# Performance work log

Measured on AMD Instinct MI355X. Metric: run time of the kernel, lower is better.

The kernel has to match this reference:

```python
import jax, jax.numpy as jnp
import numpy as np
from jax import lax

B, C, HW = 8, 512, 32
NH = 8            # num_heads
NG = 32           # num_groups
HD = C // NH      # head_size = 64
EPS = 1e-6


def group_norm(x, gamma, beta, groups=NG, eps=EPS):
    b, c, h, w = x.shape
    xr = x.reshape(b, groups, c // groups, h, w)
    mu = xr.mean(axis=(2, 3, 4), keepdims=True)
    var = xr.var(axis=(2, 3, 4), keepdims=True)
    xn = ((xr - mu) / jnp.sqrt(var + eps)).reshape(b, c, h, w)
    return xn * gamma[None, :, None, None] + beta[None, :, None, None]


def conv2d(x, w, b):
    y = lax.conv_general_dilated(x, w, (1, 1), 'SAME',
                                 dimension_numbers=('NCHW', 'OIHW', 'NCHW'))
    return y + b[None, :, None, None]


def setup_inputs() -> dict:
    key = jax.random.key(0)
    ks = jax.random.split(key, 24)
    f32 = jnp.float32

    def lin(k, out_d, in_d):
        return (jax.random.normal(k, (out_d, in_d), f32) / np.sqrt(in_d)).astype(f32)

    inp = {
        'hidden_states': jax.random.normal(ks[0], (B, C, HW, HW), f32),
        'pre_g': jnp.ones(C, f32), 'pre_b': jnp.zeros(C, f32),
        'norm_g': jnp.ones(C, f32), 'norm_b': jnp.zeros(C, f32),
        'post_g': jnp.ones(C, f32), 'post_b': jnp.zeros(C, f32),
        'pos_emb': jax.random.normal(ks[1], (1, C, 32, 32), f32) * 0.02,
        'sa_w1': (jax.random.normal(ks[2], (C // 8, C, 1, 1), f32) / np.sqrt(C)),
        'sa_b1': jnp.zeros(C // 8, f32),
        'sa_w2': (jax.random.normal(ks[3], (C // 8, C // 8, 3, 3), f32) / np.sqrt(9 * C // 8)),
        'sa_b2': jnp.zeros(C // 8, f32),
        'sa_w3': (jax.random.normal(ks[4], (1, C // 8, 1, 1), f32) / np.sqrt(C // 8)),
        'sa_b3': jnp.zeros(1, f32),
        'wq': lin(ks[5], C, C), 'wk': lin(ks[6], C, C), 'wv': lin(ks[7], C, C),
        'wq0': lin(ks[8], C // 2, C), 'wk0': lin(ks[9], C // 2, C), 'wv0': lin(ks[10], C // 2, C),
        'wq1': lin(ks[11], C // 2, C), 'wk1': lin(ks[12], C // 2, C), 'wv1': lin(ks[13], C // 2, C),
        'ff_w1': lin(ks[14], C, 2 * C), 'ff_b1': jnp.zeros(C, f32),
        'ff_w2': lin(ks[15], C, C), 'ff_b2': jnp.zeros(C, f32),
        'out_w': lin(ks[16], C, C), 'out_b': jnp.zeros(C, f32),
    }
    return inp


def reference(hidden_states, pre_g, pre_b, norm_g, norm_b, post_g, post_b,
              pos_emb, sa_w1, sa_b1, sa_w2, sa_b2, sa_w3, sa_b3,
              wq, wk, wv, wq0, wk0, wv0, wq1, wk1, wv1,
              ff_w1, ff_b1, ff_w2, ff_b2, out_w, out_b):
    b, c, h, w = hidden_states.shape
    S = h * w
    residual = hidden_states

    hs = group_norm(hidden_states, pre_g, pre_b)
    # H=W=32 matches pos_embedding; bilinear resize to same size is identity
    hs = hs + pos_emb

    # spatial attention gating (conv 1x1 -> SiLU -> conv 3x3 -> SiLU -> conv 1x1 -> sigmoid)
    a = jax.nn.silu(conv2d(hs, sa_w1, sa_b1))
    a = jax.nn.silu(conv2d(a, sa_w2, sa_b2))
    spatial_weights = jax.nn.sigmoid(conv2d(a, sa_w3, sa_b3))
    spatial_enhanced = hs * spatial_weights

    # standard multi-head self-attention over flattened tokens
    sh = group_norm(hs, norm_g, norm_b).reshape(b, c, S).transpose(0, 2, 1)  # (B,S,C)
    ehs = sh  # encoder_hidden_states defaults to standard_hidden

    q = (sh @ wq.T).reshape(b, S, NH, HD)
    k = (ehs @ wk.T).reshape(b, S, NH, HD)
    v = (ehs @ wv.T).reshape(b, S, NH, HD)
    scores = jnp.einsum('bqhd,bkhd->bhqk', q, k) / np.sqrt(HD)
    probs = jax.nn.softmax(scores, axis=-1)
    std_out = jnp.einsum('bhqk,bkhd->bqhd', probs, v).reshape(b, S, c)

    # two multi-scale single-head attention branches (dim C/2 each)
    msh = spatial_enhanced.reshape(b, c, S).transpose(0, 2, 1)  # (B,S,C)
    parts = []
    for wqm, wkm, wvm in ((wq0, wk0, wv0), (wq1, wk1, wv1)):
        qm = msh @ wqm.T          # (B,S,C/2)
        km = ehs @ wkm.T
        vm = ehs @ wvm.T
        sc = jnp.einsum('bqd,bkd->bqk', qm, km) / np.sqrt(c // 2)
        parts.append(jnp.einsum('bqk,bkd->bqd', jax.nn.softmax(sc, axis=-1), vm))
    multi_out = jnp.concatenate(parts, axis=-1)  # (B,S,C)

    combined = jnp.concatenate([std_out, multi_out], axis=-1)  # (B,S,2C)
    fused = jax.nn.silu(combined @ ff_w1.T + ff_b1) @ ff_w2.T + ff_b2  # dropout = eval identity
    final = fused @ out_w.T + out_b
    final = final.transpose(0, 2, 1).reshape(b, c, h, w)
    final = group_norm(final, post_g, post_b)
    return final + residual
```

## Files before the change

kernel.cpp:

```cpp
#include <hip/hip_runtime.h>
#include <hip/hip_bf16.h>
#include <math.h>

typedef __attribute__((ext_vector_type(8))) __bf16 v8bf;
typedef __attribute__((ext_vector_type(4))) float v4f;

__device__ __forceinline__ unsigned short f2bf(float f) {
  union { float f; unsigned int u; } a; a.f = f;
  unsigned int r = a.u + 0x7fffu + ((a.u >> 16) & 1u);
  return (unsigned short)(r >> 16);
}
__device__ __forceinline__ unsigned short f2bf_trunc(float f) {
  union { float f; unsigned int u; } a; a.f = f;
  return (unsigned short)(a.u >> 16);
}
__device__ __forceinline__ float bf2f(unsigned short u) {
  union { unsigned int i; float f; } a; a.i = ((unsigned int)u) << 16; return a.f;
}
__device__ __forceinline__ float sigm(float x) { return 1.0f / (1.0f + __expf(-x)); }

__device__ __forceinline__ void async16(const void* g, void* l) {
  __builtin_amdgcn_global_load_lds(
      (const __attribute__((address_space(1))) unsigned int*)g,
      (__attribute__((address_space(3))) unsigned int*)l, 16, 0, 0);
}

__global__ __launch_bounds__(256) void gn_pre_kernel(
    const float* __restrict__ x, const float* __restrict__ g, const float* __restrict__ be,
    const float* __restrict__ pos, unsigned short* __restrict__ hsb, float* __restrict__ stats) {
  __shared__ float L[16384];
  __shared__ float rs[4], rs2[4], mr[2];
  int b = blockIdx.x >> 5, grp = blockIdx.x & 31;
  const float4* base = (const float4*)(x + ((size_t)b*512 + grp*16)*1024);
  float4* L4 = (float4*)L;
  int w = threadIdx.x >> 6;
  float s = 0.f, s2 = 0.f;
  for (int i = threadIdx.x; i < 4096; i += 256) {
    float4 v = base[i];
    L4[i] = v;
    s += v.x + v.y + v.z + v.w;
    s2 += v.x*v.x + v.y*v.y + v.z*v.z + v.w*v.w;
  }
#pragma unroll
  for (int o = 32; o; o >>= 1) { s += __shfl_xor(s, o); s2 += __shfl_xor(s2, o); }
  if ((threadIdx.x & 63) == 0) { rs[w] = s; rs2[w] = s2; }
  __syncthreads();
  if (threadIdx.x == 0) {
    float ts = rs[0]+rs[1]+rs[2]+rs[3], ts2 = rs2[0]+rs2[1]+rs2[2]+rs2[3];
    float mu = ts * (1.0f/16384.0f);
    float var = ts2 * (1.0f/16384.0f) - mu*mu;
    mr[0] = mu; mr[1] = rsqrtf(var + 1e-6f);
  }
  __syncthreads();
  float mu = mr[0], rstd = mr[1];
  const float4* pb = (const float4*)(pos + (size_t)grp*16*1024);
  float ns = 0.f, ns2 = 0.f;
  for (int i = threadIdx.x; i < 4096; i += 256) {
    float4 v = L4[i], p = pb[i];
    int c = grp*16 + (i >> 8);
    float gg = g[c], bb = be[c];
    float4 o;
    o.x = (v.x - mu)*rstd*gg + bb + p.x;
    o.y = (v.y - mu)*rstd*gg + bb + p.y;
    o.z = (v.z - mu)*rstd*gg + bb + p.z;
    o.w = (v.w - mu)*rstd*gg + bb + p.w;
    L4[i] = o;
    ns += o.x + o.y + o.z + o.w;
    ns2 += o.x*o.x + o.y*o.y + o.z*o.z + o.w*o.w;
  }
#pragma unroll
  for (int o = 32; o; o >>= 1) { ns += __shfl_xor(ns, o); ns2 += __shfl_xor(ns2, o); }
  if ((threadIdx.x & 63) == 0) { rs[w] = ns; rs2[w] = ns2; }
  __syncthreads();
  if (threadIdx.x == 0) {
    float ts = rs[0]+rs[1]+rs[2]+rs[3], ts2 = rs2[0]+rs2[1]+rs2[2]+rs2[3];
    float nmu = ts * (1.0f/16384.0f);
    float nvar = ts2 * (1.0f/16384.0f) - nmu*nmu;
    stats[(b*32+grp)*2] = nmu; stats[(b*32+grp)*2+1] = rsqrtf(nvar + 1e-6f);
  }
#pragma unroll
  for (int j = 0; j < 4; ++j) {
    int sI = threadIdx.x + j*256;
    unsigned int wd[8];
#pragma unroll
    for (int c = 0; c < 8; ++c) {
      unsigned int lo = f2bf(L[(2*c)*1024 + sI]);
      unsigned int hi = f2bf(L[(2*c+1)*1024 + sI]);
      wd[c] = lo | (hi << 16);
    }
    size_t oo = (size_t)(b*1024 + sI)*512 + grp*16;
    *(uint4*)(hsb + oo)     = make_uint4(wd[0], wd[1], wd[2], wd[3]);
    *(uint4*)(hsb + oo + 8) = make_uint4(wd[4], wd[5], wd[6], wd[7]);
  }
}

__global__ __launch_bounds__(256) void im2col_kernel(
    const unsigned short* __restrict__ a1, unsigned short* __restrict__ im2) {
  int row0 = blockIdx.x * 8;
#pragma unroll
  for (int it = 0; it < 3; ++it) {
    int cc = it*256 + threadIdx.x;
    if (cc >= 576) break;
    int rl = cc / 72, rr = cc - rl*72;
    int tap = rr >> 3, ch8 = rr & 7;
    int row = row0 + rl;
    int bb = row >> 10, s = row & 1023;
    int y = s >> 5, xx0 = s & 31;
    int yy = y + tap/3 - 1, xx = xx0 + tap%3 - 1;
    ushort4 v0 = make_ushort4(0,0,0,0), v1 = make_ushort4(0,0,0,0);
    if ((unsigned)yy < 32u && (unsigned)xx < 32u) {
      const unsigned short* src = a1 + ((size_t)(bb*1024 + yy*32 + xx))*64 + ch8*8;
      v0 = *(const ushort4*)src; v1 = *(const ushort4*)(src + 4);
    }
    unsigned short* dst = im2 + (size_t)row*576 + tap*64 + ch8*8;
    *(ushort4*)dst = v0; *(ushort4*)(dst + 4) = v1;
  }
}

__global__ __launch_bounds__(256) void gate_norm_kernel(
    const unsigned short* __restrict__ hsb, const unsigned short* __restrict__ a2,
    const float* __restrict__ w3, const float* __restrict__ b3,
    const float* __restrict__ stats, const float* __restrict__ g,
    const float* __restrict__ be,
    unsigned short* __restrict__ sh, unsigned short* __restrict__ msh) {
  int b = blockIdx.y;
  int s = blockIdx.x * 4 + (threadIdx.x >> 6);
  int oct = threadIdx.x & 63;
  int c0 = oct * 8;
  int grp = c0 >> 4;
  float part = bf2f(a2[((size_t)(b*1024) + s)*64 + oct]) * w3[oct];
#pragma unroll
  for (int o = 32; o; o >>= 1) part += __shfl_xor(part, o);
  float wgt = sigm(part + b3[0]);
  float mu = stats[(b*32 + grp)*2], rstd = stats[(b*32 + grp)*2 + 1];
  size_t o = (size_t)(b*1024 + s)*512 + c0;
  ushort4 u0 = *(const ushort4*)(hsb + o), u1 = *(const ushort4*)(hsb + o + 4);
  unsigned short uu[8] = {u0.x,u0.y,u0.z,u0.w,u1.x,u1.y,u1.z,u1.w};
  unsigned short so[8], mo[8];
#pragma unroll
  for (int j = 0; j < 8; ++j) {
    float v = bf2f(uu[j]);
    so[j] = f2bf((v - mu)*rstd*g[c0+j] + be[c0+j]);
    mo[j] = f2bf(v * wgt);
  }
  *(ushort4*)(sh + o)     = make_ushort4(so[0], so[1], so[2], so[3]);
  *(ushort4*)(sh + o + 4) = make_ushort4(so[4], so[5], so[6], so[7]);
  *(ushort4*)(msh + o)     = make_ushort4(mo[0], mo[1], mo[2], mo[3]);
  *(ushort4*)(msh + o + 4) = make_ushort4(mo[4], mo[5], mo[6], mo[7]);
}

struct WCvt { const float* src; int dstOff; int n; float scale; };
struct WCvtArgs { WCvt w[14]; };
__global__ __launch_bounds__(256) void wconvert_kernel(WCvtArgs a, unsigned short* __restrict__ dst) {
  WCvt e = a.w[blockIdx.y];
  int i = blockIdx.x * 256 + threadIdx.x;
  if (i >= e.n) return;
  if (blockIdx.y == 13) {
    int oc = i / 576, r = i - oc*576;
    int tap = r >> 6, ic = r & 63;
    dst[e.dstOff + i] = f2bf(e.src[(oc*64 + ic)*9 + tap]);
  } else {
    dst[e.dstOff + i] = f2bf(e.src[i] * e.scale);
  }
}

__global__ __launch_bounds__(256) void transpose2_kernel(
    const unsigned short* __restrict__ qkvm,
    unsigned short* __restrict__ vtb, unsigned short* __restrict__ vmt) {
  __shared__ unsigned short t[64][65];
  int s0 = blockIdx.x * 64, c0 = blockIdx.y * 64;
  int z = blockIdx.z, b = z & 7;
  const unsigned short* in = qkvm + (z >= 8 ? 2048 : 1024);
  unsigned short* out = (z >= 8) ? vmt : vtb;
  int tx = threadIdx.x & 63, ty = threadIdx.x >> 6;
#pragma unroll
  for (int i = 0; i < 16; ++i) {
    int s = ty + i*4;
    t[s][tx] = in[((size_t)(b*1024 + s0 + s))*2560 + c0 + tx];
  }
  __syncthreads();
#pragma unroll
  for (int i = 0; i < 16; ++i) {
    int c = ty + i*4;
    out[((size_t)b*512 + c0 + c)*1024 + s0 + tx] = t[tx][c];
  }
}

struct GemmDesc {
  const unsigned short* A; const unsigned short* B; void* out; const float* bias;
  int M, N, K, lda, ldb, ldo, epi;
  long long Ay, Az, By, Bz, Oy, Oz;
};

template<int BM, int BN>
__global__ __launch_bounds__(256) void gemm_tile_kernel(GemmDesc d) {
  constexpr int WGM = (BN >= 128) ? 2 : 4;
  constexpr int WGN = 4 / WGM;
  constexpr int MT = BM / (16 * WGM);
  constexpr int NT = BN / (16 * WGN);
  constexpr int AIT = (BM * 4) / 256;
  constexpr int BIT = (BN * 4) / 256;
  __shared__ __align__(16) unsigned short As[BM * 32];
  __shared__ __align__(16) unsigned short Bs[BN * 32];

  int ntx = d.N / BN;
  int bm0 = (blockIdx.x / ntx) * BM, bn0 = (blockIdx.x % ntx) * BN;
  const unsigned short* A = d.A + (long long)blockIdx.y * d.Ay
      + (long long)blockIdx.z * d.Az + (size_t)bm0 * d.lda;
  const unsigned short* B = d.B + (long long)blockIdx.y * d.By
      + (long long)blockIdx.z * d.Bz + (size_t)bn0 * d.ldb;
  int tid = threadIdx.x, lane = tid & 63, w = tid >> 6;
  int wm = (WGN == 2) ? (w >> 1) : w;
  int wn = (WGN == 2) ? (w & 1) : 0;
  int ln = lane & 15, qd = lane >> 4;

  v4f acc[MT][NT];
#pragma unroll
  for (int i = 0; i < MT; ++i)
#pragma unroll
    for (int j = 0; j < NT; ++j) acc[i][j] = (v4f){0.f, 0.f, 0.f, 0.f};

  int nks = d.K >> 5;
  for (int ks = 0; ks < nks; ++ks) {
    int kof = ks * 32;
#pragma unroll
    for (int it = 0; it < AIT; ++it) {
      int c = it * 256 + tid;
      async16(A + (size_t)(c >> 2) * d.lda + (c & 3) * 8 + kof,
              As + (it * 256 + w * 64) * 8);
    }
#pragma unroll
    for (int it = 0; it < BIT; ++it) {
      int c = it * 256 + tid;
      async16(B + (size_t)(c >> 2) * d.ldb + (c & 3) * 8 + kof,
              Bs + (it * 256 + w * 64) * 8);
    }
    __syncthreads();
    v8bf af[MT], bfr[NT];
#pragma unroll
    for (int i = 0; i < MT; ++i)
      af[i] = *(const v8bf*)(As + (wm * MT * 16 + i * 16 + ln) * 32 + qd * 8);
#pragma unroll
    for (int j = 0; j < NT; ++j)
      bfr[j] = *(const v8bf*)(Bs + (wn * NT * 16 + j * 16 + ln) * 32 + qd * 8);
#pragma unroll
    for (int i = 0; i < MT; ++i)
#pragma unroll
      for (int j = 0; j < NT; ++j)
        acc[i][j] = __builtin_amdgcn_mfma_f32_16x16x32_bf16(af[i], bfr[j], acc[i][j], 0, 0, 0);
    __syncthreads();
  }

  size_t obase = (size_t)((long long)blockIdx.y * d.Oy + (long long)blockIdx.z * d.Oz);
#pragma unroll
  for (int i = 0; i < MT; ++i) {
#pragma unroll
    for (int j = 0; j < NT; ++j) {
      int col = bn0 + wn * NT * 16 + j * 16 + ln;
      float bia = d.bias ? d.bias[col] : 0.0f;
#pragma unroll
      for (int r = 0; r < 4; ++r) {
        int row = bm0 + wm * MT * 16 + i * 16 + qd * 4 + r;
        float v = acc[i][j][r] + bia;
        if (d.epi == 2) v = v * sigm(v);
        size_t oi = obase + (size_t)row * d.ldo + col;
        if (d.epi == 0) ((float*)d.out)[oi] = v;
        else ((unsigned short*)d.out)[oi] = f2bf(v);
      }
    }
  }
}

__global__ __launch_bounds__(256) void flash_attn_kernel(
    const unsigned short* __restrict__ QKVM, const unsigned short* __restrict__ VTB,
    unsigned short* __restrict__ out) {
  __shared__ __align__(16) unsigned short Ks[128*64];
  __shared__ __align__(16) unsigned short Vts[64*128];
  __shared__ __align__(16) unsigned short Pw[4][16*128];
  int h = blockIdx.x, b = blockIdx.y, qt = blockIdx.z;
  int tid = threadIdx.x, lane = tid & 63, w = tid >> 6;
  int ln = lane & 15, qd = lane >> 4;

  const unsigned short* Qbase = QKVM + ((size_t)(b*1024 + qt*128 + w*32))*2560 + h*64;
  v8bf aq[2][2];
#pragma unroll
  for (int i = 0; i < 2; ++i)
#pragma unroll
    for (int s = 0; s < 2; ++s)
      aq[i][s] = *(const v8bf*)(Qbase + (size_t)(i*16 + ln)*2560 + s*32 + qd*8);

  v4f o_acc[2][4];
  float l_part[2][4];
#pragma unroll
  for (int i = 0; i < 2; ++i)
#pragma unroll
    for (int dn = 0; dn < 4; ++dn) o_acc[i][dn] = (v4f){0.f,0.f,0.f,0.f};
#pragma unroll
  for (int i = 0; i < 2; ++i)
#pragma unroll
    for (int r = 0; r < 4; ++r) l_part[i][r] = 0.f;

  const unsigned short* Kg = QKVM + 512 + (size_t)(b*1024)*2560 + h*64;
  const unsigned short* Vg = VTB + ((size_t)(b*512) + h*64)*1024;

  for (int kt = 0; kt < 8; ++kt) {
#pragma unroll
    for (int it = 0; it < 4; ++it) {
      int c = it*256 + tid;
      async16(Kg + (size_t)(kt*128 + (c >> 3))*2560 + (((c & 7) ^ ((c >> 3) & 7)) << 3),
              Ks + c*8);
    }
#pragma unroll
    for (int it = 0; it < 4; ++it) {
      int c = it*256 + tid;
      async16(Vg + (size_t)(c >> 4)*1024 + kt*128 + ((((c & 15) ^ ((c >> 4) & 7))) << 3),
              Vts + c*8);
    }
    __syncthreads();

#pragma unroll
    for (int i = 0; i < 2; ++i) {
      v4f sc[8];
#pragma unroll
      for (int n = 0; n < 8; ++n) {
        v4f a = (v4f){0.f,0.f,0.f,0.f};
#pragma unroll
        for (int s = 0; s < 2; ++s) {
          v8bf kb = *(const v8bf*)(Ks + (n*16 + ln)*64 + (((s*4 + qd) ^ (ln & 7)) << 3));
          a = __builtin_amdgcn_mfma_f32_16x16x32_bf16(aq[i][s], kb, a, 0, 0, 0);
        }
        sc[n] = a;
      }
#pragma unroll
      for (int r = 0; r < 4; ++r) {
        int row7 = (qd*4 + r) & 7;
        float acc_l = 0.f;
#pragma unroll
        for (int n = 0; n < 8; ++n) {
          float p = exp2f(sc[n][r]);
          acc_l += p;
          Pw[w][(qd*4 + r)*128 + (((n*2 + (ln >> 3)) ^ row7) << 3) + (ln & 7)] = f2bf_trunc(p);
        }
        l_part[i][r] += acc_l;
      }
#pragma unroll
      for (int dn = 0; dn < 4; ++dn) {
        v4f a = o_acc[i][dn];
#pragma unroll
        for (int ks2 = 0; ks2 < 4; ++ks2) {
          int phys = (((ks2*4 + qd) ^ (ln & 7)) << 3);
          v8bf pf = *(const v8bf*)(&Pw[w][ln*128 + phys]);
          v8bf vf = *(const v8bf*)(Vts + (dn*16 + ln)*128 + phys);
          a = __builtin_amdgcn_mfma_f32_16x16x32_bf16(pf, vf, a, 0, 0, 0);
        }
        o_acc[i][dn] = a;
      }
    }
    __syncthreads();
  }

  unsigned short* ob = out + ((size_t)(b*1024 + qt*128 + w*32))*1024 + h*64;
#pragma unroll
  for (int i = 0; i < 2; ++i)
#pragma unroll
    for (int r = 0; r < 4; ++r) {
      float l = l_part[i][r];
      l += __shfl_xor(l, 1); l += __shfl_xor(l, 2);
      l += __shfl_xor(l, 4); l += __shfl_xor(l, 8);
      float rinv = 1.0f / l;
#pragma unroll
      for (int dn = 0; dn < 4; ++dn)
        ob[(size_t)(i*16 + qd*4 + r)*1024 + dn*16 + ln] = f2bf(o_acc[i][dn][r] * rinv);
    }
}

__global__ __launch_bounds__(256) void softmax_bf16_kernel(
    const unsigned short* __restrict__ S, unsigned short* __restrict__ P, int nrows) {
  int row = blockIdx.x * 4 + (threadIdx.x >> 6);
  if (row >= nrows) return;
  int l = threadIdx.x & 63;
  const ushort4* sp = (const ushort4*)(S + (size_t)row * 1024);
  float v[16];
  float m = -1e30f;
#pragma unroll
  for (int t = 0; t < 4; ++t) {
    ushort4 u = sp[t*64 + l];
    v[t*4+0] = bf2f(u.x); v[t*4+1] = bf2f(u.y); v[t*4+2] = bf2f(u.z); v[t*4+3] = bf2f(u.w);
    m = fmaxf(m, fmaxf(fmaxf(v[t*4], v[t*4+1]), fmaxf(v[t*4+2], v[t*4+3])));
  }
#pragma unroll
  for (int o = 32; o; o >>= 1) m = fmaxf(m, __shfl_xor(m, o));
  float sum = 0.f;
#pragma unroll
  for (int t = 0; t < 16; ++t) { v[t] = __expf(v[t] - m); sum += v[t]; }
#pragma unroll
  for (int o = 32; o; o >>= 1) sum += __shfl_xor(sum, o);
  float r = 1.0f / sum;
  ushort4* p = (ushort4*)(P + (size_t)row * 1024);
#pragma unroll
  for (int t = 0; t < 4; ++t)
    p[t*64 + l] = make_ushort4(f2bf_trunc(v[t*4]*r), f2bf_trunc(v[t*4+1]*r),
                               f2bf_trunc(v[t*4+2]*r), f2bf_trunc(v[t*4+3]*r));
}

__global__ __launch_bounds__(256) void gn_stats_bf16_kernel(
    const unsigned short* __restrict__ t, float* __restrict__ stats) {
  int b = blockIdx.x >> 5, grp = blockIdx.x & 31;
  float s = 0.f, s2 = 0.f;
#pragma unroll
  for (int j = 0; j < 4; ++j) {
    int sI = threadIdx.x + j*256;
    const unsigned short* p = t + ((size_t)(b*1024 + sI))*512 + grp*16;
    uint4 a = *(const uint4*)p, c2 = *(const uint4*)(p + 8);
    unsigned int ww[8] = {a.x,a.y,a.z,a.w,c2.x,c2.y,c2.z,c2.w};
#pragma unroll
    for (int k = 0; k < 8; ++k) {
      float lo = bf2f((unsigned short)(ww[k] & 0xffff));
      float hi = bf2f((unsigned short)(ww[k] >> 16));
      s += lo + hi; s2 += lo*lo + hi*hi;
    }
  }
#pragma unroll
  for (int o = 32; o; o >>= 1) { s += __shfl_xor(s, o); s2 += __shfl_xor(s2, o); }
  __shared__ float rs[4], rs2[4];
  int w = threadIdx.x >> 6;
  if ((threadIdx.x & 63) == 0) { rs[w] = s; rs2[w] = s2; }
  __syncthreads();
  if (threadIdx.x == 0) {
    float ts = rs[0]+rs[1]+rs[2]+rs[3], ts2 = rs2[0]+rs2[1]+rs2[2]+rs2[3];
    float mu = ts * (1.0f/16384.0f);
    float var = ts2 * (1.0f/16384.0f) - mu*mu;
    stats[(b*32+grp)*2] = mu; stats[(b*32+grp)*2+1] = rsqrtf(var + 1e-6f);
  }
}

__global__ __launch_bounds__(256) void final_out_kernel(
    const unsigned short* __restrict__ fin, const float* __restrict__ stats,
    const float* __restrict__ g, const float* __restrict__ be,
    const float* __restrict__ x, float* __restrict__ out) {
  __shared__ float t[64][65];
  int s0 = blockIdx.x * 64, c0 = blockIdx.y * 64, b = blockIdx.z;
  int tx = threadIdx.x & 63, ty = threadIdx.x >> 6;
#pragma unroll
  for (int i = 0; i < 16; ++i) {
    int s = ty + i*4;
    t[s][tx] = bf2f(fin[((size_t)(b*1024 + s0 + s))*512 + c0 + tx]);
  }
  __syncthreads();
#pragma unroll
  for (int i = 0; i < 16; ++i) {
    int c = ty + i*4;
    int cc = c0 + c, grp = cc >> 4;
    float mu = stats[(b*32+grp)*2], rstd = stats[(b*32+grp)*2+1];
    float gg = g[cc], bb = be[cc];
    size_t oi = ((size_t)(b*512 + cc))*1024 + s0 + tx;
    out[oi] = (t[tx][c] - mu)*rstd*gg + bb + x[oi];
  }
}

static void launch_gemm128(hipStream_t st, const unsigned short* A, const unsigned short* B,
                           void* out, const float* bias,
                           int M, int N, int K, int lda, int ldb, int ldo, int epi,
                           long long Ay, long long Az, long long By, long long Bz,
                           long long Oy, long long Oz, int gy, int gz) {
  GemmDesc d{A, B, out, bias, M, N, K, lda, ldb, ldo, epi, Ay, Az, By, Bz, Oy, Oz};
  gemm_tile_kernel<128,128><<<dim3((M/128)*(N/128), gy, gz), dim3(256), 0, st>>>(d);
}
static void launch_gemm64(hipStream_t st, const unsigned short* A, const unsigned short* B,
                          void* out, const float* bias,
                          int M, int N, int K, int lda, int ldb, int ldo, int epi) {
  GemmDesc d{A, B, out, bias, M, N, K, lda, ldb, ldo, epi, 0,0,0,0,0,0};
  gemm_tile_kernel<128,64><<<dim3((M/128)*(N/64), 1, 1), dim3(256), 0, st>>>(d);
}

extern "C" void kernel_launch(void* const* d_in, const int* in_sizes, int n_in,
                              void* d_out, int out_size, void* d_ws, size_t ws_size,
                              hipStream_t stream) {
  const float* x      = (const float*)d_in[0];
  const float* pre_g  = (const float*)d_in[1];
  const float* pre_b  = (const float*)d_in[2];
  const float* norm_g = (const float*)d_in[3];
  const float* norm_b = (const float*)d_in[4];
  const float* post_g = (const float*)d_in[5];
  const float* post_b = (const float*)d_in[6];
  const float* pos    = (const float*)d_in[7];
  const float* sa_b1  = (const float*)d_in[9];
  const float* sa_b2  = (const float*)d_in[11];
  const float* sa_w3  = (const float*)d_in[12];
  const float* sa_b3  = (const float*)d_in[13];
  const float* ff_b1  = (const float*)d_in[24];
  const float* ff_b2  = (const float*)d_in[26];
  const float* out_b  = (const float*)d_in[28];
  float* outp = (float*)d_out;

  char* ws = (char*)d_ws;
  size_t off = 0;
  auto alloc = [&](size_t bytes) -> void* {
    void* p = ws + off; off += (bytes + 255) & ~(size_t)255; return p;
  };
  float* STATS = (float*)alloc(4096);
  unsigned short* HSB  = (unsigned short*)alloc(8388608);
  unsigned short* A1   = (unsigned short*)alloc(1048576);
  unsigned short* IM2  = (unsigned short*)alloc(9437184);
  unsigned short* A2   = (unsigned short*)alloc(1048576);
  unsigned short* SHB  = (unsigned short*)alloc(8388608);
  unsigned short* MSHB = (unsigned short*)alloc(8388608);
  unsigned short* WBF  = (unsigned short*)alloc(6291456);
  unsigned short* QKVM = (unsigned short*)alloc(41943040);
  unsigned short* QM   = (unsigned short*)alloc(8388608);
  unsigned short* VTB  = (unsigned short*)alloc(8388608);
  unsigned short* VMT  = (unsigned short*)alloc(8388608);
  unsigned short* SBUF = (unsigned short*)alloc(16777216);
  unsigned short* PBUF = (unsigned short*)alloc(16777216);
  unsigned short* COMB = (unsigned short*)alloc(16777216);
  unsigned short* FFMID= (unsigned short*)alloc(8388608);
  unsigned short* FUSED= (unsigned short*)alloc(8388608);
  unsigned short* FINALB=(unsigned short*)alloc(8388608);

  const int OQKVM=0, OQM=1310720, OFF1=1572864, OFF2=2097152,
            OOW=2359296, OW1=2621440, OW2R=2654208;

  gn_pre_kernel<<<dim3(256), dim3(256), 0, stream>>>(x, pre_g, pre_b, pos, HSB, STATS);
  {
    WCvtArgs a;
    const float LG2E = 1.4426950408889634f;
    const int   srcIdx[14] = {14,15,16, 18,21,19,22, 17,20, 23,25,27, 8, 10};
    const int   dofs[14]   = {0, 262144, 524288,
                              786432, 917504, 1048576, 1179648,
                              OQM, OQM+131072,
                              OFF1, OFF2, OOW, OW1, OW2R};
    const int   ns[14]     = {262144,262144,262144, 131072,131072,131072,131072,
                              131072,131072, 524288,262144,262144, 32768, 36864};
    const float sc[14]     = {0.125f*LG2E,1.f,1.f, 1.f,1.f,1.f,1.f,
                              0.0625f,0.0625f, 1.f,1.f,1.f, 1.f, 1.f};
    for (int i = 0; i < 14; ++i) { a.w[i].src = (const float*)d_in[srcIdx[i]]; a.w[i].dstOff = dofs[i]; a.w[i].n = ns[i]; a.w[i].scale = sc[i]; }
    wconvert_kernel<<<dim3(2048, 14), dim3(256), 0, stream>>>(a, WBF);
  }
  launch_gemm64(stream, HSB, WBF+OW1,  A1, sa_b1, 8192, 64, 512, 512, 512, 64, 2);
  im2col_kernel<<<dim3(1024), dim3(256), 0, stream>>>(A1, IM2);
  launch_gemm64(stream, IM2, WBF+OW2R, A2, sa_b2, 8192, 64, 576, 576, 576, 64, 2);
  gate_norm_kernel<<<dim3(256, 8), dim3(256), 0, stream>>>(HSB, A2, sa_w3, sa_b3, STATS, norm_g, norm_b, SHB, MSHB);

  launch_gemm128(stream, SHB,  WBF+OQKVM, QKVM, nullptr, 8192, 2560, 512, 512, 512, 2560, 1, 0,0,0,0,0,0, 1,1);
  launch_gemm128(stream, MSHB, WBF+OQM,   QM,   nullptr, 8192, 512,  512, 512, 512, 512,  1, 0,0,0,0,0,0, 1,1);

  transpose2_kernel<<<dim3(16, 8, 16), dim3(256), 0, stream>>>(QKVM, VTB, VMT);

  flash_attn_kernel<<<dim3(8, 8, 8), dim3(256), 0, stream>>>(QKVM, VTB, COMB);

  for (int br = 0; br < 2; ++br) {
    launch_gemm128(stream, QM + br*256, QKVM + 1536 + br*256, SBUF, nullptr,
                   1024, 1024, 256, 512, 2560, 1024, 1,
                   1024LL*512, 0, 1024LL*2560, 0, 1024LL*1024, 0, 8, 1);
    softmax_bf16_kernel<<<dim3(2048), dim3(256), 0, stream>>>(SBUF, PBUF, 8192);
    launch_gemm128(stream, PBUF, VMT + (size_t)br*256*1024, COMB + 512 + br*256, nullptr,
                   1024, 256, 1024, 1024, 1024, 1024, 1,
                   1024LL*1024, 0, 512LL*1024, 0, 1024LL*1024, 0, 8, 1);
  }

  launch_gemm128(stream, COMB,  WBF+OFF1, FFMID,  ff_b1, 8192, 512, 1024, 1024, 1024, 512, 2, 0,0,0,0,0,0, 1,1);
  launch_gemm128(stream, FFMID, WBF+OFF2, FUSED,  ff_b2, 8192, 512, 512,  512,  512,  512, 1, 0,0,0,0,0,0, 1,1);
  launch_gemm128(stream, FUSED, WBF+OOW,  FINALB, out_b, 8192, 512, 512,  512,  512,  512, 1, 0,0,0,0,0,0, 1,1);

  gn_stats_bf16_kernel<<<dim3(256), dim3(256), 0, stream>>>(FINALB, STATS);
  final_out_kernel<<<dim3(16, 8, 8), dim3(256), 0, stream>>>(FINALB, STATS, post_g, post_b, x, outp);

  (void)in_sizes; (void)n_in; (void)out_size; (void)ws_size;
}
```

Measured before the change: 479.9 us.

## Fold ff_w2 and out_w into one weight, batch attention branches, XCD-aware tile mapping

Precomputes out_w·ff_w2 as a combined 512x512 weight and a folded bias, so the two back-to-back linear layers become a single GEMM over the activations. The two multi-scale attention branches are launched as one batched GEMM/softmax/GEMM sequence via the z grid dimension instead of a loop, halving launches. GEMM tiles are remapped so consecutive blocks on the same XCD share M rows for better L2 locality. This adds a small per-call weight GEMM, a bias kernel and larger score buffers, and the folded weight is rounded to bf16 once more.

Measured after the change: 457.3 us. -4.7%, faster.

```diff
diff --git a/kernel.cpp b/kernel.cpp
--- a/kernel.cpp
+++ b/kernel.cpp
@@ -150,7 +150,7 @@
 }
 
 struct WCvt { const float* src; int dstOff; int n; float scale; };
-struct WCvtArgs { WCvt w[14]; };
+struct WCvtArgs { WCvt w[15]; };
 __global__ __launch_bounds__(256) void wconvert_kernel(WCvtArgs a, unsigned short* __restrict__ dst) {
   WCvt e = a.w[blockIdx.y];
   int i = blockIdx.x * 256 + threadIdx.x;
@@ -159,9 +159,22 @@
     int oc = i / 576, r = i - oc*576;
     int tap = r >> 6, ic = r & 63;
     dst[e.dstOff + i] = f2bf(e.src[(oc*64 + ic)*9 + tap]);
+  } else if (blockIdx.y == 14) {
+    dst[e.dstOff + i] = f2bf(e.src[(i & 511)*512 + (i >> 9)]);
   } else {
     dst[e.dstOff + i] = f2bf(e.src[i] * e.scale);
   }
+}
+
+__global__ __launch_bounds__(256) void bias_fold_kernel(
+    const float* __restrict__ ow, const float* __restrict__ b2,
+    const float* __restrict__ ob, float* __restrict__ bc) {
+  int n = blockIdx.x * 256 + threadIdx.x;
+  float s = ob[n];
+  const float* r = ow + (size_t)n * 512;
+#pragma unroll 8
+  for (int j = 0; j < 512; ++j) s += r[j] * b2[j];
+  bc[n] = s;
 }
 
 __global__ __launch_bounds__(256) void transpose2_kernel(
@@ -203,8 +216,17 @@
   __shared__ __align__(16) unsigned short As[BM * 32];
   __shared__ __align__(16) unsigned short Bs[BN * 32];
 
-  int ntx = d.N / BN;
-  int bm0 = (blockIdx.x / ntx) * BM, bn0 = (blockIdx.x % ntx) * BN;
+  int ntx = d.N / BN, mtx = d.M / BM;
+  int bmt, bnt;
+  if ((mtx & 7) == 0) {
+    int xcd = blockIdx.x & 7, j = blockIdx.x >> 3;
+    int mpx = mtx >> 3;
+    bmt = xcd * mpx + (j % mpx);
+    bnt = j / mpx;
+  } else {
+    bmt = blockIdx.x / ntx; bnt = blockIdx.x % ntx;
+  }
+  int bm0 = bmt * BM, bn0 = bnt * BN;
   const unsigned short* A = d.A + (long long)blockIdx.y * d.Ay
       + (long long)blockIdx.z * d.Az + (size_t)bm0 * d.lda;
   const unsigned short* B = d.B + (long long)blockIdx.y * d.By
@@ -490,6 +512,7 @@
   const float* sa_b3  = (const float*)d_in[13];
   const float* ff_b1  = (const float*)d_in[24];
   const float* ff_b2  = (const float*)d_in[26];
+  const float* out_w  = (const float*)d_in[27];
   const float* out_b  = (const float*)d_in[28];
   float* outp = (float*)d_out;
 
@@ -499,6 +522,7 @@
     void* p = ws + off; off += (bytes + 255) & ~(size_t)255; return p;
   };
   float* STATS = (float*)alloc(4096);
+  float* BC    = (float*)alloc(2048);
   unsigned short* HSB  = (unsigned short*)alloc(8388608);
   unsigned short* A1   = (unsigned short*)alloc(1048576);
   unsigned short* IM2  = (unsigned short*)alloc(9437184);
@@ -506,36 +530,41 @@
   unsigned short* SHB  = (unsigned short*)alloc(8388608);
   unsigned short* MSHB = (unsigned short*)alloc(8388608);
   unsigned short* WBF  = (unsigned short*)alloc(6291456);
+  unsigned short* WCOMB= (unsigned short*)alloc(524288);
   unsigned short* QKVM = (unsigned short*)alloc(41943040);
   unsigned short* QM   = (unsigned short*)alloc(8388608);
   unsigned short* VTB  = (unsigned short*)alloc(8388608);
   unsigned short* VMT  = (unsigned short*)alloc(8388608);
-  unsigned short* SBUF = (unsigned short*)alloc(16777216);
-  unsigned short* PBUF = (unsigned short*)alloc(16777216);
+  unsigned short* SBUF = (unsigned short*)alloc(33554432);
+  unsigned short* PBUF = (unsigned short*)alloc(33554432);
   unsigned short* COMB = (unsigned short*)alloc(16777216);
   unsigned short* FFMID= (unsigned short*)alloc(8388608);
-  unsigned short* FUSED= (unsigned short*)alloc(8388608);
   unsigned short* FINALB=(unsigned short*)alloc(8388608);
 
-  const int OQKVM=0, OQM=1310720, OFF1=1572864, OFF2=2097152,
+  const int OQKVM=0, OQM=1310720, OFF1=1572864, OFF2T=2097152,
             OOW=2359296, OW1=2621440, OW2R=2654208;
 
   gn_pre_kernel<<<dim3(256), dim3(256), 0, stream>>>(x, pre_g, pre_b, pos, HSB, STATS);
   {
     WCvtArgs a;
     const float LG2E = 1.4426950408889634f;
-    const int   srcIdx[14] = {14,15,16, 18,21,19,22, 17,20, 23,25,27, 8, 10};
-    const int   dofs[14]   = {0, 262144, 524288,
+    const int   srcIdx[15] = {14,15,16, 18,21,19,22, 17,20, 23,27, 8, 0 , 10, 25};
+    const int   dofs[15]   = {0, 262144, 524288,
                               786432, 917504, 1048576, 1179648,
                               OQM, OQM+131072,
-                              OFF1, OFF2, OOW, OW1, OW2R};
-    const int   ns[14]     = {262144,262144,262144, 131072,131072,131072,131072,
-                              131072,131072, 524288,262144,262144, 32768, 36864};
-    const float sc[14]     = {0.125f*LG2E,1.f,1.f, 1.f,1.f,1.f,1.f,
-                              0.0625f,0.0625f, 1.f,1.f,1.f, 1.f, 1.f};
-    for (int i = 0; i < 14; ++i) { a.w[i].src = (const float*)d_in[srcIdx[i]]; a.w[i].dstOff = dofs[i]; a.w[i].n = ns[i]; a.w[i].scale = sc[i]; }
-    wconvert_kernel<<<dim3(2048, 14), dim3(256), 0, stream>>>(a, WBF);
-  }
+                              OFF1, OOW, OW1, 0, OW2R, OFF2T};
+    const int   ns[15]     = {262144,262144,262144, 131072,131072,131072,131072,
+                              131072,131072, 524288,262144, 32768, 0, 36864, 262144};
+    const float sc[15]     = {0.125f*LG2E,1.f,1.f, 1.f,1.f,1.f,1.f,
+                              0.0625f,0.0625f, 1.f,1.f, 1.f, 0.f, 1.f, 1.f};
+    for (int i = 0; i < 15; ++i) { a.w[i].src = (const float*)d_in[srcIdx[i]]; a.w[i].dstOff = dofs[i]; a.w[i].n = ns[i]; a.w[i].scale = sc[i]; }
+    wconvert_kernel<<<dim3(2048, 15), dim3(256), 0, stream>>>(a, WBF);
+  }
+  {
+    GemmDesc d{WBF+OOW, WBF+OFF2T, WCOMB, nullptr, 512, 512, 512, 512, 512, 512, 1, 0,0,0,0,0,0};
+    gemm_tile_kernel<128,128><<<dim3(16, 1, 1), dim3(256), 0, stream>>>(d);
+  }
+  bias_fold_kernel<<<dim3(2), dim3(256), 0, stream>>>(out_w, ff_b2, out_b, BC);
   launch_gemm64(stream, HSB, WBF+OW1,  A1, sa_b1, 8192, 64, 512, 512, 512, 64, 2);
   im2col_kernel<<<dim3(1024), dim3(256), 0, stream>>>(A1, IM2);
   launch_gemm64(stream, IM2, WBF+OW2R, A2, sa_b2, 8192, 64, 576, 576, 576, 64, 2);
@@ -548,19 +577,16 @@
 
   flash_attn_kernel<<<dim3(8, 8, 8), dim3(256), 0, stream>>>(QKVM, VTB, COMB);
 
-  for (int br = 0; br < 2; ++br) {
-    launch_gemm128(stream, QM + br*256, QKVM + 1536 + br*256, SBUF, nullptr,
-                   1024, 1024, 256, 512, 2560, 1024, 1,
-                   1024LL*512, 0, 1024LL*2560, 0, 1024LL*1024, 0, 8, 1);
-    softmax_bf16_kernel<<<dim3(2048), dim3(256), 0, stream>>>(SBUF, PBUF, 8192);
-    launch_gemm128(stream, PBUF, VMT + (size_t)br*256*1024, COMB + 512 + br*256, nullptr,
-                   1024, 256, 1024, 1024, 1024, 1024, 1,
-                   1024LL*1024, 0, 512LL*1024, 0, 1024LL*1024, 0, 8, 1);
-  }
+  launch_gemm128(stream, QM, QKVM + 1536, SBUF, nullptr,
+                 1024, 1024, 256, 512, 2560, 1024, 1,
+                 1024LL*512, 256, 1024LL*2560, 256, 1024LL*1024, 8388608, 8, 2);
+  softmax_bf16_kernel<<<dim3(4096), dim3(256), 0, stream>>>(SBUF, PBUF, 16384);
+  launch_gemm128(stream, PBUF, VMT, COMB + 512, nullptr,
+                 1024, 256, 1024, 1024, 1024, 1024, 1,
+                 1024LL*1024, 8388608, 512LL*1024, 256LL*1024, 1024LL*1024, 256, 8, 2);
 
   launch_gemm128(stream, COMB,  WBF+OFF1, FFMID,  ff_b1, 8192, 512, 1024, 1024, 1024, 512, 2, 0,0,0,0,0,0, 1,1);
-  launch_gemm128(stream, FFMID, WBF+OFF2, FUSED,  ff_b2, 8192, 512, 512,  512,  512,  512, 1, 0,0,0,0,0,0, 1,1);
-  launch_gemm128(stream, FUSED, WBF+OOW,  FINALB, out_b, 8192, 512, 512,  512,  512,  512, 1, 0,0,0,0,0,0, 1,1);
+  launch_gemm128(stream, FFMID, WCOMB,    FINALB, BC,    8192, 512, 512,  512,  512,  512, 1, 0,0,0,0,0,0, 1,1);
 
   gn_stats_bf16_kernel<<<dim3(256), dim3(256), 0, stream>>>(FINALB, STATS);
   final_out_kernel<<<dim3(16, 8, 8), dim3(256), 0, stream>>>(FINALB, STATS, post_g, post_b, x, outp);
```
